# Performance work log

Measured on AMD Instinct MI355X. Metric: run time of the kernel, lower is better.

Reference implementation:

```python
import jax, jax.numpy as jnp
import numpy as np

EPS = 1e-20  # MaskSoftmax epsilon
S, T, B, H, V = 64, 64, 128, 1024, 32000


def _attn(s, h, u, mask, sa_w, sa_b, a1_w, a1_b):
    # Bahdanau attention with mask-softmax over the source (dim 0)
    t = jnp.tanh(s @ sa_w + sa_b + u)               # [S,B,H]
    e = jnp.einsum('sbh,h->sb', t, a1_w) + a1_b     # [S,B]
    x = jnp.exp(e - jnp.max(e, axis=0, keepdims=True)) * mask
    alpha = x / (jnp.sum(x, axis=0, keepdims=True) + EPS)
    return jnp.einsum('sb,sbh->bh', alpha, h)       # [B,H]


def _gru(x, h, ym, W, U, b, C=None, c=None):
    xg = x @ W + b
    if C is not None:
        xg = xg + c @ C
    hg = h @ U
    xz, xr, xh = jnp.split(xg, 3, axis=-1)
    hz, hr, hh = jnp.split(hg, 3, axis=-1)
    z = jax.nn.sigmoid(xz + hz)
    r = jax.nn.sigmoid(xr + hr)
    hn = (1.0 - z) * h + z * jnp.tanh(xh + r * hh)
    m = ym[:, None]
    return m * hn + (1.0 - m) * h


def _forward(ys, xs_h, uh, xs_mask, ys_mask, s_tm1, emb, sa_w, sa_b, a1_w, a1_b,
             ha_w, ha_b, W1, U1, b1, W2, U2, C2, b2,
             ua1_w, ua1_b, ua2_w, ua2_b, ls_w, ls_b, ly_w, ly_b, lc_w, lc_b):
    ys_e = emb[ys]                                              # [T,B,H]
    btg_uh = jnp.einsum('sbh,hk->sbk', xs_h, ha_w) + ha_b        # [S,B,H]

    def step(s, inp):
        y_e, ym = inp
        s_above = _gru(y_e, s, ym, W1, U1, b1)                   # gru1
        a1 = _attn(s_above, xs_h, uh, xs_mask, sa_w, sa_b, a1_w, a1_b)
        a2 = _attn(s_above, xs_h, btg_uh, xs_mask, sa_w, sa_b, a1_w, a1_b)
        s_t = _gru(a1, s_above, ym, W2, U2, b2, C2, a2)          # gru2 with extra ctx
        g = jax.nn.sigmoid(a1 @ ua1_w + ua1_b + a2 @ ua2_w + ua2_b)
        att = g * a1 + (1.0 - g) * a2                            # gated fusion
        logit = s_t @ ls_w + ls_b + y_e @ ly_w + ly_b + att @ lc_w + lc_b  # [B,2H]
        logit = jnp.max(logit.reshape(logit.shape[0], -1, 2), axis=-1)     # maxout
        return s_t, logit

    _, logits = jax.lax.scan(step, s_tm1, (ys_e, ys_mask))       # [T,B,H]
    return logits * ys_mask[:, :, None]


def setup_inputs():
    key = jax.random.key(0)
    ks = jax.random.split(key, 20)
    rn = lambda k, sh, s=0.02: jax.random.normal(k, sh, jnp.float32) * s
    inp = {}
    inp['ys'] = jax.random.randint(ks[0], (T, B), 0, V)
    inp['xs_h'] = jax.random.normal(ks[1], (S, B, H), jnp.float32)
    inp['uh'] = jax.random.normal(ks[2], (S, B, H), jnp.float32)
    inp['xs_mask'] = jnp.ones((S, B), jnp.float32)
    inp['ys_mask'] = jnp.ones((T, B), jnp.float32)
    inp['s_tm1'] = rn(ks[3], (B, H), 1.0)
    emb = rn(ks[4], (V, H), 1.0)
    inp['emb'] = emb.at[0].set(0.0)  # padding_idx = 0
    inp['sa_w'] = rn(ks[5], (H, H)); inp['sa_b'] = jnp.zeros((H,), jnp.float32)
    inp['a1_w'] = rn(ks[6], (H,));   inp['a1_b'] = jnp.zeros((), jnp.float32)
    inp['ha_w'] = rn(ks[7], (H, H)); inp['ha_b'] = jnp.zeros((H,), jnp.float32)
    inp['W1'] = rn(ks[8], (H, 3 * H)); inp['U1'] = rn(ks[9], (H, 3 * H)); inp['b1'] = jnp.zeros((3 * H,), jnp.float32)
    inp['W2'] = rn(ks[10], (H, 3 * H)); inp['U2'] = rn(ks[11], (H, 3 * H)); inp['C2'] = rn(ks[12], (H, 3 * H)); inp['b2'] = jnp.zeros((3 * H,), jnp.float32)
    inp['ua1_w'] = rn(ks[13], (H, H)); inp['ua1_b'] = jnp.zeros((H,), jnp.float32)
    inp['ua2_w'] = rn(ks[14], (H, H)); inp['ua2_b'] = jnp.zeros((H,), jnp.float32)
    inp['ls_w'] = rn(ks[15], (H, 2 * H)); inp['ls_b'] = jnp.zeros((2 * H,), jnp.float32)
    inp['ly_w'] = rn(ks[16], (H, 2 * H)); inp['ly_b'] = jnp.zeros((2 * H,), jnp.float32)
    inp['lc_w'] = rn(ks[17], (H, 2 * H)); inp['lc_b'] = jnp.zeros((2 * H,), jnp.float32)
    return inp


def reference(ys, xs_h, uh, xs_mask, ys_mask, s_tm1, emb, sa_w, sa_b, a1_w, a1_b,
              ha_w, ha_b, W1, U1, b1, W2, U2, C2, b2,
              ua1_w, ua1_b, ua2_w, ua2_b, ls_w, ls_b, ly_w, ly_b, lc_w, lc_b):
    return _forward(ys, xs_h, uh, xs_mask, ys_mask, s_tm1, emb, sa_w, sa_b, a1_w, a1_b,
                    ha_w, ha_b, W1, U1, b1, W2, U2, C2, b2,
                    ua1_w, ua1_b, ua2_w, ua2_b, ls_w, ls_b, ly_w, ly_b, lc_w, lc_b)
```

## Files before the change

kernel.cpp:

```cpp
#include <hip/hip_runtime.h>
#include <hip/hip_bf16.h>
#include <cstddef>
#include <cstdint>

#define Sdim 64
#define Tdim 64
#define Bdim 128
#define Hdim 1024
#define H3 3072
#define TB (Tdim * Bdim)
#define SB (Sdim * Bdim)
#define NWG 256

typedef __attribute__((ext_vector_type(4))) float f32x4;
typedef __attribute__((ext_vector_type(8))) short bf16x8;

__device__ __forceinline__ float rcpf(float x) { return __builtin_amdgcn_rcpf(x); }
__device__ __forceinline__ float sigf(float x) { return rcpf(1.0f + __expf(-x)); }
__device__ __forceinline__ float tanh_fast(float x) {
  x = fminf(fmaxf(x, -15.0f), 15.0f);
  float t = __expf(2.0f * x);
  return (t - 1.0f) * rcpf(t + 1.0f);
}
__device__ __forceinline__ float bl(uint32_t u) { return __uint_as_float(u << 16); }
__device__ __forceinline__ float bh(uint32_t u) { return __uint_as_float(u & 0xffff0000u); }
__device__ __forceinline__ float b2f(uint16_t v) { return __uint_as_float((uint32_t)v << 16); }
__device__ __forceinline__ uint16_t f2b(float f) {
  __hip_bfloat16 h = __float2bfloat16(f);
  return *reinterpret_cast<uint16_t*>(&h);
}

__device__ __forceinline__ uint32_t ald32(const void* p) {
  return __hip_atomic_load((const uint32_t*)p, __ATOMIC_RELAXED, __HIP_MEMORY_SCOPE_AGENT);
}
__device__ __forceinline__ unsigned long long ald64(const void* p) {
  return __hip_atomic_load((const unsigned long long*)p, __ATOMIC_RELAXED, __HIP_MEMORY_SCOPE_AGENT);
}
__device__ __forceinline__ void ast32(void* p, uint32_t v) {
  __hip_atomic_store((uint32_t*)p, v, __ATOMIC_RELAXED, __HIP_MEMORY_SCOPE_AGENT);
}
__device__ __forceinline__ void ast64(void* p, unsigned long long v) {
  __hip_atomic_store((unsigned long long*)p, v, __ATOMIC_RELAXED, __HIP_MEMORY_SCOPE_AGENT);
}
__device__ __forceinline__ float aldf(const void* p) { return __uint_as_float(ald32(p)); }
__device__ __forceinline__ void astf(void* p, float v) { ast32(p, __float_as_uint(v)); }
__device__ __forceinline__ uint4 ald128(const void* p) {
  unsigned long long a = ald64(p);
  unsigned long long b = ald64((const char*)p + 8);
  uint4 r;
  r.x = (uint32_t)a; r.y = (uint32_t)(a >> 32);
  r.z = (uint32_t)b; r.w = (uint32_t)(b >> 32);
  return r;
}

struct MDesc {
  const uint16_t* A0; const uint16_t* B0;
  const uint16_t* A1; const uint16_t* B1;
  const uint16_t* A2; const uint16_t* B2;
  const float* bias0; const float* bias1; const float* bias2;
  float* C;
  int M, N, K;
};

template<int BM, int BN, int MODE>
__global__ __launch_bounds__(256) void mgemm(MDesc d, const float* __restrict__ ymask,
                                             float* __restrict__ outp)
{
  const int nb = blockIdx.x * BN;
  const int mb = blockIdx.y * BM;
  if (nb >= d.N || mb >= d.M) return;

  __shared__ char lds[(BM + BN) * 128];
  char* As = lds;
  char* Bs = lds + BM * 128;

  const int t = threadIdx.x;
  const int lane = t & 63;
  const int wid = t >> 6;
  const int wm = wid >> 1, wn = wid & 1;
  constexpr int WM = BM / 2, WN = BN / 2;
  constexpr int MR = WM / 16, NR = WN / 16;
  constexpr int CA = BM / 32;
  constexpr int CB = BN / 32;

  const int arow_base = wm * WM + (lane & 15);
  const int brow_base = wn * WN + (lane & 15);
  const int akb = (lane >> 4) * 16;
  const int axA = (arow_base & 7) << 4;
  const int axB = (brow_base & 7) << 4;

  f32x4 acc[MR][NR];
  #pragma unroll
  for (int m = 0; m < MR; ++m)
    #pragma unroll
    for (int n = 0; n < NR; ++n)
      acc[m][n] = (f32x4){0.f, 0.f, 0.f, 0.f};

  const int K = d.K;
  const int nkt = K / 64;

  #pragma unroll 1
  for (int p = 0; p < 3; ++p) {
    const uint16_t* A = (p == 0) ? d.A0 : (p == 1 ? d.A1 : d.A2);
    const uint16_t* B = (p == 0) ? d.B0 : (p == 1 ? d.B1 : d.B2);
    if (A == nullptr) break;

    const char* gA[CA]; int lA[CA];
    const char* gB[CB]; int lB[CB];
    #pragma unroll
    for (int c = 0; c < CA; ++c) {
      int i = c * 256 + t, row = i >> 3, kb = (i & 7) * 16;
      gA[c] = (const char*)A + (size_t)(mb + row) * K * 2 + kb;
      lA[c] = row * 128 + (kb ^ ((row & 7) << 4));
    }
    #pragma unroll
    for (int c = 0; c < CB; ++c) {
      int i = c * 256 + t, row = i >> 3, kb = (i & 7) * 16;
      gB[c] = (const char*)B + (size_t)(nb + row) * K * 2 + kb;
      lB[c] = row * 128 + (kb ^ ((row & 7) << 4));
    }

    uint4 ra[CA], rb[CB];
    #pragma unroll
    for (int c = 0; c < CA; ++c) ra[c] = *(const uint4*)gA[c];
    #pragma unroll
    for (int c = 0; c < CB; ++c) rb[c] = *(const uint4*)gB[c];

    for (int kk = 0; kk < nkt; ++kk) {
      __syncthreads();
      #pragma unroll
      for (int c = 0; c < CA; ++c) *(uint4*)(As + lA[c]) = ra[c];
      #pragma unroll
      for (int c = 0; c < CB; ++c) *(uint4*)(Bs + lB[c]) = rb[c];
      __syncthreads();
      if (kk + 1 < nkt) {
        #pragma unroll
        for (int c = 0; c < CA; ++c) ra[c] = *(const uint4*)(gA[c] + (size_t)(kk + 1) * 128);
        #pragma unroll
        for (int c = 0; c < CB; ++c) rb[c] = *(const uint4*)(gB[c] + (size_t)(kk + 1) * 128);
      }
      #pragma unroll
      for (int ks = 0; ks < 2; ++ks) {
        bf16x8 av[MR], bv[NR];
        #pragma unroll
        for (int m = 0; m < MR; ++m) {
          int row = arow_base + m * 16;
          av[m] = *(const bf16x8*)(As + row * 128 + ((ks * 64 + akb) ^ axA));
        }
        #pragma unroll
        for (int n = 0; n < NR; ++n) {
          int row = brow_base + n * 16;
          bv[n] = *(const bf16x8*)(Bs + row * 128 + ((ks * 64 + akb) ^ axB));
        }
        #pragma unroll
        for (int m = 0; m < MR; ++m)
          #pragma unroll
          for (int n = 0; n < NR; ++n)
            acc[m][n] = __builtin_amdgcn_mfma_f32_16x16x32_bf16(av[m], bv[n], acc[m][n], 0, 0, 0);
      }
    }
  }

  const int cm = (lane >> 4) * 4;
  const int cn = lane & 15;
  #pragma unroll
  for (int n = 0; n < NR; ++n) {
    int col = nb + wn * WN + n * 16 + cn;
    float bias = 0.f;
    if (d.bias0) bias += d.bias0[col];
    if (d.bias1) bias += d.bias1[col];
    if (d.bias2) bias += d.bias2[col];
    #pragma unroll
    for (int m = 0; m < MR; ++m) {
      #pragma unroll
      for (int j = 0; j < 4; ++j) {
        int row = mb + wm * WM + m * 16 + cm + j;
        float v = acc[m][n][j] + bias;
        if (MODE == 1) {
          ((uint16_t*)d.C)[(size_t)row * d.N + col] = f2b(v);
        } else {
          float o = __shfl_xor(v, 1);
          if (!(lane & 1))
            outp[(size_t)row * (d.N / 2) + (col >> 1)] = fmaxf(v, o) * ymask[row];
        }
      }
    }
  }
}

static inline MDesc mk(const uint16_t* A0, const uint16_t* B0,
                       const uint16_t* A1, const uint16_t* B1,
                       const uint16_t* A2, const uint16_t* B2,
                       const float* b0, const float* b1, const float* b2,
                       float* C, int M, int N, int K)
{
  MDesc d;
  d.A0 = A0; d.B0 = B0; d.A1 = A1; d.B1 = B1; d.A2 = A2; d.B2 = B2;
  d.bias0 = b0; d.bias1 = b1; d.bias2 = b2;
  d.C = C; d.M = M; d.N = N; d.K = K;
  return d;
}

__global__ __launch_bounds__(256) void transpose_bf16_k(const float* __restrict__ in,
                                                        uint16_t* __restrict__ out,
                                                        int K, int N)
{
  __shared__ float tile[32][33];
  int nx = blockIdx.x * 32, ky = blockIdx.y * 32;
  int tx = threadIdx.x & 31, ty = threadIdx.x >> 5;
  #pragma unroll
  for (int i = 0; i < 4; ++i)
    tile[ty + i * 8][tx] = in[(size_t)(ky + ty + i * 8) * N + nx + tx];
  __syncthreads();
  #pragma unroll
  for (int i = 0; i < 4; ++i)
    out[(size_t)(nx + ty + i * 8) * K + ky + tx] = f2b(tile[tx][ty + i * 8]);
}

__global__ __launch_bounds__(256) void ptranspose_k(const float* __restrict__ in,
                                                    uint16_t* __restrict__ out,
                                                    int K, int N)
{
  __shared__ float tile[32][33];
  int nx = blockIdx.x * 32, ky = blockIdx.y * 32;
  int tx = threadIdx.x & 31, ty = threadIdx.x >> 5;
  #pragma unroll
  for (int i = 0; i < 4; ++i)
    tile[ty + i * 8][tx] = in[(size_t)(ky + ty + i * 8) * N + nx + tx];
  __syncthreads();
  #pragma unroll
  for (int i = 0; i < 4; ++i) {
    int n = nx + ty + i * 8;
    int h = n & 1023, g = n >> 10;
    int np = (h >> 4) * 48 + g * 16 + (h & 15);
    out[(size_t)np * K + ky + tx] = f2b(tile[tx][ty + i * 8]);
  }
}

__global__ __launch_bounds__(256) void pack_k(const float* __restrict__ b1,
                                              const float* __restrict__ b2,
                                              float* __restrict__ b1p,
                                              float* __restrict__ b2p,
                                              int* __restrict__ bar)
{
  int i = blockIdx.x * 256 + threadIdx.x;
  if (i < 1024) bar[i] = 0;
  if (i < H3) {
    int g = (i >> 4) % 3, hblk = i / 48, hi = i & 15;
    int n = g * 1024 + hblk * 16 + hi;
    b1p[i] = b1[n];
    b2p[i] = b2[n];
  }
}

__global__ __launch_bounds__(256) void cvt_bf16_k(const float* __restrict__ in,
                                                  uint16_t* __restrict__ out)
{
  int gid = blockIdx.x * 256 + threadIdx.x;
  float4 v = ((const float4*)in)[gid];
  uint2 o;
  o.x = (uint32_t)f2b(v.x) | ((uint32_t)f2b(v.y) << 16);
  o.y = (uint32_t)f2b(v.z) | ((uint32_t)f2b(v.w) << 16);
  ((uint2*)out)[gid] = o;
}

__global__ __launch_bounds__(256) void embed_k(const int* __restrict__ ys,
                                               const float* __restrict__ emb,
                                               uint16_t* __restrict__ ys_e)
{
  int gid = blockIdx.x * 256 + threadIdx.x;
  int h4 = gid & 255;
  int tb = gid >> 8;
  int tok = ys[tb];
  float4 v = ((const float4*)emb)[(size_t)tok * 256 + h4];
  uint2 o;
  o.x = (uint32_t)f2b(v.x) | ((uint32_t)f2b(v.y) << 16);
  o.y = (uint32_t)f2b(v.z) | ((uint32_t)f2b(v.w) << 16);
  ((uint2*)ys_e)[gid] = o;
}

struct ScanArgs {
  const uint16_t *U1p, *W2p, *C2p, *U2p;
  const uint16_t *sawt, *ua1t, *ua2t;
  const uint16_t *xw1p;
  const uint16_t *uh_bf, *btg_bf, *xs_bf;
  const uint16_t *stm1_bf;
  const float *s_tm1, *ys_mask, *xs_mask, *a1w, *a1b, *sa_b;
  const float *b2p, *ua1_b, *ua2_b;
  float *sf0, *sf1, *sab_f, *qbuf, *e1, *e2, *c1f, *c2f, *ahg;
  uint16_t *sab_bf, *c1b, *c2b, *shist_bf, *att_bf;
  int *bar;
};

__device__ __forceinline__ void gsync(int* bar, int gen, int wg) {
  __syncthreads();
  if (threadIdx.x == 0) {
    asm volatile("s_waitcnt vmcnt(0)" ::: "memory");
    int old = __hip_atomic_fetch_add(bar + (wg & 15) * 32, 1,
                                     __ATOMIC_RELAXED, __HIP_MEMORY_SCOPE_AGENT);
    if (old == gen * 16 - 1) {
      int ro = __hip_atomic_fetch_add(bar + 512, 1,
                                      __ATOMIC_RELAXED, __HIP_MEMORY_SCOPE_AGENT);
      if (ro == gen * 16 - 1)
        __hip_atomic_store(bar + 544, gen, __ATOMIC_RELAXED, __HIP_MEMORY_SCOPE_AGENT);
    }
    while (__hip_atomic_load(bar + 544, __ATOMIC_RELAXED, __HIP_MEMORY_SCOPE_AGENT) < gen)
      __builtin_amdgcn_s_sleep(2);
    asm volatile("s_waitcnt vmcnt(0)" ::: "memory");
  }
  __syncthreads();
}

#define HS1 16384
#define HS2 12288
#define HS6 16384
#define HS5 32768

__global__ __launch_bounds__(256, 1) void scan2_k(ScanArgs a) {
  const int wg = blockIdx.x;
  const int t = threadIdx.x;
  const int lane = t & 63, w = t >> 6;
  const int r15 = lane & 15;
  const int akb = (lane >> 4) * 16;
  __shared__ char lds[64 * 1024];
  int gen = 0;

  float wv[16];
  {
    const float* wp = a.a1w + lane * 16;
    #pragma unroll
    for (int j = 0; j < 16; ++j) wv[j] = wp[j];
  }
  const float abv = a.a1b[0];

  const int b34 = wg & 127;
  const uint16_t* src34 = (wg < 128) ? a.uh_bf : a.btg_bf;
  const size_t s34_base = ((size_t)(w * 16) * Bdim + b34) * 1024 + lane * 16;
  float* cf34 = (wg < 128) ? a.c1f : a.c2f;
  uint16_t* cb34 = (wg < 128) ? a.c1b : a.c2b;
  const uint16_t* xp34 = a.xs_bf + (size_t)b34 * 1024 + t * 4;

  const int bh6 = (wg & 127) >> 6, hb6 = wg & 63;
  const char* ga6[4]; int la6[4];
  {
    #pragma unroll
    for (int c = 0; c < 4; ++c) {
      int i = c * 256 + t;
      int row = i >> 3, kb = (i & 7) * 16;
      if (i < 512) {
        ga6[c] = (const char*)a.sab_bf + ((size_t)(bh6 * 64 + row) * 1024) * 2 + kb;
      } else if (i < 896) {
        int j2 = i - 512; int row2 = j2 >> 3;
        ga6[c] = (const char*)a.U2p + ((size_t)(hb6 * 48 + row2) * 1024) * 2 + kb;
        row = 64 + row2;
      } else {
        ga6[c] = (const char*)a.U2p + kb;
      }
      la6[c] = row * 128 + (kb ^ ((row & 7) << 4));
    }
  }

  const int bh5 = (wg & 127) >> 6, hblk = wg & 63;
  const char* ga5[8]; int la5[8];
  {
    #pragma unroll
    for (int c = 0; c < 8; ++c) {
      int i = c * 256 + t;
      int kb = (i & 7) * 16, grow = i >> 3;
      const char* gp;
      if (grow < 64)       gp = (const char*)a.c1b  + ((size_t)(bh5 * 64 + grow)        * 1024) * 2;
      else if (grow < 128) gp = (const char*)a.c2b  + ((size_t)(bh5 * 64 + grow - 64)   * 1024) * 2;
      else if (grow < 176) gp = (const char*)a.W2p  + ((size_t)(hblk * 48 + grow - 128) * 1024) * 2;
      else if (grow < 224) gp = (const char*)a.C2p  + ((size_t)(hblk * 48 + grow - 176) * 1024) * 2;
      else if (grow < 240) gp = (const char*)a.ua1t + ((size_t)(hblk * 16 + grow - 224) * 1024) * 2;
      else                 gp = (const char*)a.ua2t + ((size_t)(hblk * 16 + grow - 240) * 1024) * 2;
      ga5[c] = gp + kb;
      la5[c] = grow * 128 + (kb ^ ((grow & 7) << 4));
    }
  }

  for (int step = 0; step < Tdim; ++step) {
    const uint16_t* sprev_bf = step ? (a.shist_bf + (size_t)(step - 1) * Bdim * Hdim) : a.stm1_bf;
    const float* sprev_f = (step == 0) ? a.s_tm1 : ((step & 1) ? a.sf0 : a.sf1);
    float* snext_f = (step & 1) ? a.sf1 : a.sf0;
    const float* ymt = a.ys_mask + (size_t)step * Bdim;
    uint16_t* shist_t = a.shist_bf + (size_t)step * Bdim * Hdim;
    uint16_t* att_t = a.att_bf + (size_t)step * Bdim * Hdim;
    const uint16_t* xw1t = a.xw1p + (size_t)step * Bdim * H3;

    uint4 v6w0, v6w1, v6w2, v6w3;

    if (wg < 128) {
      const char* ga1[4]; int la1[4];
      #pragma unroll
      for (int c = 0; c < 4; ++c) {
        int i = c * 256 + t;
        int row = i >> 3, kb = (i & 7) * 16;
        if (i < 512) {
          ga1[c] = (const char*)sprev_bf + ((size_t)(bh5 * 64 + row) * 1024) * 2 + kb;
        } else if (i < 896) {
          int j2 = i - 512; int row2 = j2 >> 3;
          ga1[c] = (const char*)a.U1p + ((size_t)(hblk * 48 + row2) * 1024) * 2 + kb;
          row = 64 + row2;
        } else {
          ga1[c] = (const char*)a.U1p + kb;
        }
        la1[c] = row * 128 + (kb ^ ((row & 7) << 4));
      }
      f32x4 ac0 = {0.f,0.f,0.f,0.f}, ac1 = ac0, ac2 = ac0;
      const int arow = w * 16 + r15;
      const int axA = (arow & 7) << 4;
      const int axB = (r15 & 7) << 4;
      uint4 rA[4], rB[4];
      auto ld1 = [&](uint4* r, int tile) {
        #pragma unroll
        for (int c = 0; c < 4; ++c)
          r[c] = (c < 2) ? ald128(ga1[c] + (size_t)tile * 128)
                         : *(const uint4*)(ga1[c] + (size_t)tile * 128);
      };
      auto st1 = [&](const uint4* r, int half) {
        char* base = lds + half * HS1;
        #pragma unroll
        for (int c = 0; c < 4; ++c) *(uint4*)(base + la1[c]) = r[c];
      };
      auto cp1 = [&](int half) {
        const char* base = lds + half * HS1;
        #pragma unroll
        for (int ks = 0; ks < 2; ++ks) {
          int ko = ks * 64 + akb;
          bf16x8 av = *(const bf16x8*)(base + arow * 128 + (ko ^ axA));
          bf16x8 b0 = *(const bf16x8*)(base + (64 + r15) * 128 + (ko ^ axB));
          bf16x8 b1 = *(const bf16x8*)(base + (80 + r15) * 128 + (ko ^ axB));
          bf16x8 b2 = *(const bf16x8*)(base + (96 + r15) * 128 + (ko ^ axB));
          ac0 = __builtin_amdgcn_mfma_f32_16x16x32_bf16(av, b0, ac0, 0, 0, 0);
          ac1 = __builtin_amdgcn_mfma_f32_16x16x32_bf16(av, b1, ac1, 0, 0, 0);
          ac2 = __builtin_amdgcn_mfma_f32_16x16x32_bf16(av, b2, ac2, 0, 0, 0);
        }
      };
      ld1(rA, 0); ld1(rB, 1);
      st1(rA, 0);
      #pragma unroll 1
      for (int kk2 = 0; kk2 < 8; ++kk2) {
        __syncthreads();
        st1(rB, 1);
        if (kk2 < 7) ld1(rA, 2 * kk2 + 2);
        cp1(0);
        __syncthreads();
        if (kk2 < 7) { st1(rA, 0); ld1(rB, 2 * kk2 + 3); }
        cp1(1);
      }
      const int hgl = hblk * 16 + r15;
      const int bbase = bh5 * 64 + w * 16 + ((lane >> 4) << 2);
      #pragma unroll
      for (int j = 0; j < 4; ++j) {
        int b = bbase + j;
        size_t xr_ = (size_t)b * H3 + hblk * 48 + r15;
        float xz = b2f(xw1t[xr_]);
        float xr = b2f(xw1t[xr_ + 16]);
        float xh = b2f(xw1t[xr_ + 32]);
        float hp = aldf(sprev_f + b * 1024 + hgl);
        float z = sigf(xz + ac0[j]);
        float r = sigf(xr + ac1[j]);
        float hn = (1.f - z) * hp + z * tanh_fast(xh + r * ac2[j]);
        float m = ymt[b];
        float o = m * hn + (1.f - m) * hp;
        astf(a.sab_f + b * 1024 + hgl, o);
        uint32_t me = f2b(o);
        uint32_t other = (uint32_t)__shfl_xor((int)me, 1);
        if (!(lane & 1))
          ast32((char*)a.sab_bf + ((size_t)b * 1024 + hgl) * 2, me | (other << 16));
      }
    } else {
      v6w0 = *(const uint4*)ga6[2];
      v6w1 = *(const uint4*)ga6[3];
      v6w2 = *(const uint4*)(ga6[2] + 128);
      v6w3 = *(const uint4*)(ga6[3] + 128);
    }
    gsync(a.bar, ++gen, wg);

    if (wg < 64) {
      const int bh2 = wg >> 5, nblk = wg & 31;
      const char* ga2[3]; int la2[3];
      #pragma unroll
      for (int c = 0; c < 3; ++c) {
        int i = c * 256 + t;
        int row, kb = (i & 7) * 16;
        if (i < 512) {
          row = i >> 3;
          ga2[c] = (const char*)a.sab_bf + ((size_t)(bh2 * 64 + row) * 1024) * 2 + kb;
        } else {
          int j2 = i - 512; int row2 = j2 >> 3;
          ga2[c] = (const char*)a.sawt + ((size_t)(nblk * 32 + row2) * 1024) * 2 + kb;
          row = 64 + row2;
        }
        la2[c] = row * 128 + (kb ^ ((row & 7) << 4));
      }
      f32x4 q0 = {0.f,0.f,0.f,0.f}, q1 = q0;
      const int arow = w * 16 + r15;
      const int axA = (arow & 7) << 4;
      const int axB = (r15 & 7) << 4;
      uint4 rA[3], rB[3];
      auto ld2 = [&](uint4* r, int tile) {
        #pragma unroll
        for (int c = 0; c < 3; ++c)
          r[c] = (c < 2) ? ald128(ga2[c] + (size_t)tile * 128)
                         : *(const uint4*)(ga2[c] + (size_t)tile * 128);
      };
      auto st2 = [&](const uint4* r, int half) {
        char* base = lds + half * HS2;
        #pragma unroll
        for (int c = 0; c < 3; ++c) *(uint4*)(base + la2[c]) = r[c];
      };
      auto cp2 = [&](int half) {
        const char* base = lds + half * HS2;
        #pragma unroll
        for (int ks = 0; ks < 2; ++ks) {
          int ko = ks * 64 + akb;
          bf16x8 av = *(const bf16x8*)(base + arow * 128 + (ko ^ axA));
          bf16x8 b0 = *(const bf16x8*)(base + (64 + r15) * 128 + (ko ^ axB));
          bf16x8 b1 = *(const bf16x8*)(base + (80 + r15) * 128 + (ko ^ axB));
          q0 = __builtin_amdgcn_mfma_f32_16x16x32_bf16(av, b0, q0, 0, 0, 0);
          q1 = __builtin_amdgcn_mfma_f32_16x16x32_bf16(av, b1, q1, 0, 0, 0);
        }
      };
      ld2(rA, 0); ld2(rB, 1);
      st2(rA, 0);
      #pragma unroll 1
      for (int kk2 = 0; kk2 < 8; ++kk2) {
        __syncthreads();
        st2(rB, 1);
        if (kk2 < 7) ld2(rA, 2 * kk2 + 2);
        cp2(0);
        __syncthreads();
        if (kk2 < 7) { st2(rA, 0); ld2(rB, 2 * kk2 + 3); }
        cp2(1);
      }
      #pragma unroll
      for (int n = 0; n < 2; ++n) {
        int col = nblk * 32 + n * 16 + r15;
        float sb = a.sa_b[col];
        #pragma unroll
        for (int j = 0; j < 4; ++j) {
          int b = bh2 * 64 + w * 16 + ((lane >> 4) << 2) + j;
          astf(a.qbuf + b * 1024 + col, (n ? q1[j] : q0[j]) + sb);
        }
      }
    } else if (wg >= 128) {
      f32x4 ac0 = {0.f,0.f,0.f,0.f}, ac1 = ac0, ac2 = ac0;
      const int arow = w * 16 + r15;
      const int axA = (arow & 7) << 4;
      const int axB = (r15 & 7) << 4;
      uint4 rA[4], rB[4];
      auto ld6 = [&](uint4* r, int tile) {
        #pragma unroll
        for (int c = 0; c < 4; ++c)
          r[c] = (c < 2) ? ald128(ga6[c] + (size_t)tile * 128)
                         : *(const uint4*)(ga6[c] + (size_t)tile * 128);
      };
      auto st6 = [&](const uint4* r, int half) {
        char* base = lds + half * HS6;
        #pragma unroll
        for (int c = 0; c < 4; ++c) *(uint4*)(base + la6[c]) = r[c];
      };
      auto cp6 = [&](int half) {
        const char* base = lds + half * HS6;
        #pragma unroll
        for (int ks = 0; ks < 2; ++ks) {
          int ko = ks * 64 + akb;
          bf16x8 av = *(const bf16x8*)(base + arow * 128 + (ko ^ axA));
          bf16x8 b0 = *(const bf16x8*)(base + (64 + r15) * 128 + (ko ^ axB));
          bf16x8 b1 = *(const bf16x8*)(base + (80 + r15) * 128 + (ko ^ axB));
          bf16x8 b2 = *(const bf16x8*)(base + (96 + r15) * 128 + (ko ^ axB));
          ac0 = __builtin_amdgcn_mfma_f32_16x16x32_bf16(av, b0, ac0, 0, 0, 0);
          ac1 = __builtin_amdgcn_mfma_f32_16x16x32_bf16(av, b1, ac1, 0, 0, 0);
          ac2 = __builtin_amdgcn_mfma_f32_16x16x32_bf16(av, b2, ac2, 0, 0, 0);
        }
      };
      rA[0] = ald128(ga6[0]);       rA[1] = ald128(ga6[1]);
      rA[2] = v6w0;                 rA[3] = v6w1;
      rB[0] = ald128(ga6[0] + 128); rB[1] = ald128(ga6[1] + 128);
      rB[2] = v6w2;                 rB[3] = v6w3;
      st6(rA, 0);
      #pragma unroll 1
      for (int kk2 = 0; kk2 < 8; ++kk2) {
        __syncthreads();
        st6(rB, 1);
        if (kk2 < 7) ld6(rA, 2 * kk2 + 2);
        cp6(0);
        __syncthreads();
        if (kk2 < 7) { st6(rA, 0); ld6(rB, 2 * kk2 + 3); }
        cp6(1);
      }
      const int bbase6 = bh6 * 64 + w * 16 + ((lane >> 4) << 2);
      #pragma unroll
      for (int j = 0; j < 4; ++j) {
        int b = bbase6 + j;
        float* ap = a.ahg + (size_t)b * H3 + hb6 * 48 + r15;
        astf(ap, ac0[j]);
        astf(ap + 16, ac1[j]);
        astf(ap + 32, ac2[j]);
      }
    }
    uint4 pa0 = *(const uint4*)(src34 + s34_base);
    uint4 pa1 = *(const uint4*)(src34 + s34_base + 8);
    gsync(a.bar, ++gen, wg);

    {
      float* e_lds = (float*)lds;
      float qv[16];
      const float* qp = a.qbuf + (size_t)b34 * 1024 + lane * 16;
      #pragma unroll
      for (int k2 = 0; k2 < 8; ++k2) {
        unsigned long long q2 = ald64(qp + k2 * 2);
        qv[2 * k2]     = __uint_as_float((uint32_t)q2);
        qv[2 * k2 + 1] = __uint_as_float((uint32_t)(q2 >> 32));
      }
      auto score = [&](uint4 u0, uint4 u1, int si) {
        float pv = 0.f;
        uint32_t uu[8] = {u0.x,u0.y,u0.z,u0.w,u1.x,u1.y,u1.z,u1.w};
        #pragma unroll
        for (int k = 0; k < 8; ++k) {
          pv += wv[2*k]   * tanh_fast(qv[2*k]   + bl(uu[k]));
          pv += wv[2*k+1] * tanh_fast(qv[2*k+1] + bh(uu[k]));
        }
        #pragma unroll
        for (int off = 32; off > 0; off >>= 1) pv += __shfl_xor(pv, off);
        if (lane == 0) e_lds[w * 16 + si] = pv + abv;
      };
      uint4 pb0, pb1;
      {
        const uint16_t* np = src34 + s34_base + (size_t)Bdim * 1024;
        pb0 = *(const uint4*)np; pb1 = *(const uint4*)(np + 8);
      }
      #pragma unroll 1
      for (int s2 = 0; s2 < 8; ++s2) {
        {
          int si = 2 * s2;
          uint4 u0 = pa0, u1 = pa1;
          if (s2 < 7) {
            const uint16_t* np = src34 + s34_base + (size_t)(si + 2) * Bdim * 1024;
            pa0 = *(const uint4*)np; pa1 = *(const uint4*)(np + 8);
          }
          score(u0, u1, si);
        }
        {
          int si = 2 * s2 + 1;
          uint4 u0 = pb0, u1 = pb1;
          if (s2 < 7) {
            const uint16_t* np = src34 + s34_base + (size_t)(si + 2) * Bdim * 1024;
            pb0 = *(const uint4*)np; pb1 = *(const uint4*)(np + 8);
          }
          score(u0, u1, si);
        }
      }
      __syncthreads();
      if (w == 0) {
        float vv = e_lds[lane];
        float mx = vv;
        #pragma unroll
        for (int off = 32; off > 0; off >>= 1) mx = fmaxf(mx, __shfl_xor(mx, off));
        float x = __expf(vv - mx) * a.xs_mask[lane * Bdim + b34];
        float sm = x;
        #pragma unroll
        for (int off = 32; off > 0; off >>= 1) sm += __shfl_xor(sm, off);
        e_lds[lane] = x * rcpf(sm + 1e-20f);
      }
      __syncthreads();
      float s0 = 0.f, s1 = 0.f, s2 = 0.f, s3 = 0.f;
      #pragma unroll 8
      for (int s = 0; s < Sdim; ++s) {
        unsigned long long u = *(const unsigned long long*)(xp34 + (size_t)s * Bdim * 1024);
        float aa = e_lds[s];
        s0 += aa * bl((uint32_t)u);
        s1 += aa * bh((uint32_t)u);
        s2 += aa * bl((uint32_t)(u >> 32));
        s3 += aa * bh((uint32_t)(u >> 32));
      }
      size_t o = (size_t)b34 * 1024 + t * 4;
      ast64(cf34 + o,     (unsigned long long)__float_as_uint(s0)
                        | ((unsigned long long)__float_as_uint(s1) << 32));
      ast64(cf34 + o + 2, (unsigned long long)__float_as_uint(s2)
                        | ((unsigned long long)__float_as_uint(s3) << 32));
      unsigned long long pb = (unsigned long long)f2b(s0)
                            | ((unsigned long long)f2b(s1) << 16)
                            | ((unsigned long long)f2b(s2) << 32)
                            | ((unsigned long long)f2b(s3) << 48);
      ast64((char*)cb34 + o * 2, pb);
    }
    uint4 v5w[8];
    if (wg < 128) {
      #pragma unroll
      for (int c = 4; c < 8; ++c) {
        v5w[c - 4] = *(const uint4*)ga5[c];
        v5w[c]     = *(const uint4*)(ga5[c] + 128);
      }
    }
    gsync(a.bar, ++gen, wg);

    if (wg < 128) {
      f32x4 ax0 = {0.f,0.f,0.f,0.f}, ax1 = ax0, ax2 = ax0, ag = ax0;
      uint4 rA[8], rB[8];
      auto ld5 = [&](uint4* r, int tile) {
        #pragma unroll
        for (int c = 0; c < 8; ++c)
          r[c] = (c < 4) ? ald128(ga5[c] + (size_t)tile * 128)
                         : *(const uint4*)(ga5[c] + (size_t)tile * 128);
      };
      auto st5 = [&](const uint4* r, int half) {
        char* base = lds + half * HS5;
        #pragma unroll
        for (int c = 0; c < 8; ++c) *(uint4*)(base + la5[c]) = r[c];
      };
      auto cp5 = [&](int half) {
        const char* base = lds + half * HS5;
        #pragma unroll
        for (int ks = 0; ks < 2; ++ks) {
          const int ko = ks * 64 + akb;
          #define LD(row_) (*(const bf16x8*)(base + (row_) * 128 + (ko ^ (((row_) & 7) << 4))))
          bf16x8 a1v = LD(w * 16 + r15);
          bf16x8 a2v = LD(64 + w * 16 + r15);
          bf16x8 bw0 = LD(128 + r15), bw1 = LD(144 + r15), bw2 = LD(160 + r15);
          bf16x8 bc0 = LD(176 + r15), bc1 = LD(192 + r15), bc2 = LD(208 + r15);
          bf16x8 g1v = LD(224 + r15), g2v = LD(240 + r15);
          #undef LD
          ax0 = __builtin_amdgcn_mfma_f32_16x16x32_bf16(a1v, bw0, ax0, 0, 0, 0);
          ax0 = __builtin_amdgcn_mfma_f32_16x16x32_bf16(a2v, bc0, ax0, 0, 0, 0);
          ax1 = __builtin_amdgcn_mfma_f32_16x16x32_bf16(a1v, bw1, ax1, 0, 0, 0);
          ax1 = __builtin_amdgcn_mfma_f32_16x16x32_bf16(a2v, bc1, ax1, 0, 0, 0);
          ax2 = __builtin_amdgcn_mfma_f32_16x16x32_bf16(a1v, bw2, ax2, 0, 0, 0);
          ax2 = __builtin_amdgcn_mfma_f32_16x16x32_bf16(a2v, bc2, ax2, 0, 0, 0);
          ag  = __builtin_amdgcn_mfma_f32_16x16x32_bf16(a1v, g1v, ag, 0, 0, 0);
          ag  = __builtin_amdgcn_mfma_f32_16x16x32_bf16(a2v, g2v, ag, 0, 0, 0);
        }
      };
      #pragma unroll
      for (int c = 0; c < 4; ++c) {
        rA[c] = ald128(ga5[c]);
        rB[c] = ald128(ga5[c] + 128);
      }
      #pragma unroll
      for (int c = 4; c < 8; ++c) { rA[c] = v5w[c - 4]; rB[c] = v5w[c]; }
      st5(rA, 0);
      #pragma unroll 1
      for (int kk2 = 0; kk2 < 8; ++kk2) {
        __syncthreads();
        st5(rB, 1);
        if (kk2 < 7) ld5(rA, 2 * kk2 + 2);
        cp5(0);
        __syncthreads();
        if (kk2 < 7) { st5(rA, 0); ld5(rB, 2 * kk2 + 3); }
        cp5(1);
      }
      const int hgl = hblk * 16 + r15;
      float bz  = a.b2p[hblk * 48 + r15];
      float brr = a.b2p[hblk * 48 + 16 + r15];
      float bhh = a.b2p[hblk * 48 + 32 + r15];
      float gb  = a.ua1_b[hgl] + a.ua2_b[hgl];
      const int bbase = bh5 * 64 + w * 16 + ((lane >> 4) << 2);
      float ahz[4], ahr[4], ahh[4], hpv[4], c1v[4], c2v[4];
      #pragma unroll
      for (int j = 0; j < 4; ++j) {
        int b = bbase + j;
        const float* ap = a.ahg + (size_t)b * H3 + hblk * 48 + r15;
        ahz[j] = aldf(ap);
        ahr[j] = aldf(ap + 16);
        ahh[j] = aldf(ap + 32);
        hpv[j] = aldf(a.sab_f + (size_t)b * 1024 + hgl);
        c1v[j] = aldf(a.c1f + (size_t)b * 1024 + hgl);
        c2v[j] = aldf(a.c2f + (size_t)b * 1024 + hgl);
      }
      #pragma unroll
      for (int j = 0; j < 4; ++j) {
        int b = bbase + j;
        float hp = hpv[j];
        float z = sigf(ax0[j] + bz + ahz[j]);
        float r = sigf(ax1[j] + brr + ahr[j]);
        float hn = (1.f - z) * hp + z * tanh_fast(ax2[j] + bhh + r * ahh[j]);
        float m = ymt[b];
        float st = m * hn + (1.f - m) * hp;
        astf(snext_f + b * 1024 + hgl, st);
        uint32_t me = f2b(st);
        uint32_t other = (uint32_t)__shfl_xor((int)me, 1);
        if (!(lane & 1))
          ast32((char*)shist_t + ((size_t)b * 1024 + hgl) * 2, me | (other << 16));
        float g = sigf(ag[j] + gb);
        float att = g * c1v[j] + (1.f - g) * c2v[j];
        att_t[(size_t)b * 1024 + hgl] = f2b(att);
      }
    }
    gsync(a.bar, ++gen, wg);
  }
}

extern "C" void kernel_launch(void* const* d_in, const int* in_sizes, int n_in,
                              void* d_out, int out_size, void* d_ws, size_t ws_size,
                              hipStream_t stream)
{
  const int*   ys      = (const int*)  d_in[0];
  const float* xs_h    = (const float*)d_in[1];
  const float* uh      = (const float*)d_in[2];
  const float* xs_mask = (const float*)d_in[3];
  const float* ys_mask = (const float*)d_in[4];
  const float* s_tm1   = (const float*)d_in[5];
  const float* emb     = (const float*)d_in[6];
  const float* sa_w    = (const float*)d_in[7];
  const float* sa_b    = (const float*)d_in[8];
  const float* a1_w    = (const float*)d_in[9];
  const float* a1_b    = (const float*)d_in[10];
  const float* ha_w    = (const float*)d_in[11];
  const float* ha_b    = (const float*)d_in[12];
  const float* W1      = (const float*)d_in[13];
  const float* U1      = (const float*)d_in[14];
  const float* b1      = (const float*)d_in[15];
  const float* W2      = (const float*)d_in[16];
  const float* U2      = (const float*)d_in[17];
  const float* C2      = (const float*)d_in[18];
  const float* b2      = (const float*)d_in[19];
  const float* ua1_w   = (const float*)d_in[20];
  const float* ua1_b   = (const float*)d_in[21];
  const float* ua2_w   = (const float*)d_in[22];
  const float* ua2_b   = (const float*)d_in[23];
  const float* ls_w    = (const float*)d_in[24];
  const float* ls_b    = (const float*)d_in[25];
  const float* ly_w    = (const float*)d_in[26];
  const float* ly_b    = (const float*)d_in[27];
  const float* lc_w    = (const float*)d_in[28];
  const float* lc_b    = (const float*)d_in[29];
  (void)in_sizes; (void)n_in; (void)out_size; (void)ws_size;

  float* out = (float*)d_out;

  char* wp = (char*)d_ws;
  auto alloc = [&](size_t bytes) { char* r = wp; wp += (bytes + 255) & ~(size_t)255; return r; };

  uint16_t* W1p  = (uint16_t*)alloc((size_t)H3 * Hdim * 2);
  uint16_t* U1p  = (uint16_t*)alloc((size_t)H3 * Hdim * 2);
  uint16_t* W2p  = (uint16_t*)alloc((size_t)H3 * Hdim * 2);
  uint16_t* U2p  = (uint16_t*)alloc((size_t)H3 * Hdim * 2);
  uint16_t* C2p  = (uint16_t*)alloc((size_t)H3 * Hdim * 2);
  uint16_t* sawt = (uint16_t*)alloc((size_t)Hdim * Hdim * 2);
  uint16_t* hawt = (uint16_t*)alloc((size_t)Hdim * Hdim * 2);
  uint16_t* ua1t = (uint16_t*)alloc((size_t)Hdim * Hdim * 2);
  uint16_t* ua2t = (uint16_t*)alloc((size_t)Hdim * Hdim * 2);
  uint16_t* lst  = (uint16_t*)alloc((size_t)2048 * Hdim * 2);
  uint16_t* lyt  = (uint16_t*)alloc((size_t)2048 * Hdim * 2);
  uint16_t* lct  = (uint16_t*)alloc((size_t)2048 * Hdim * 2);
  float* b1p = (float*)alloc((size_t)H3 * 4);
  float* b2p = (float*)alloc((size_t)H3 * 4);
  int* bar   = (int*)alloc(4096);
  uint16_t* uh_bf   = (uint16_t*)alloc((size_t)SB * Hdim * 2);
  uint16_t* xs_bf   = (uint16_t*)alloc((size_t)SB * Hdim * 2);
  uint16_t* btg_bf  = (uint16_t*)alloc((size_t)SB * Hdim * 2);
  uint16_t* ys_e_bf = (uint16_t*)alloc((size_t)TB * Hdim * 2);
  uint16_t* xw1p    = (uint16_t*)alloc((size_t)TB * H3 * 2);
  uint16_t* shist_bf= (uint16_t*)alloc((size_t)TB * Hdim * 2);
  uint16_t* att_bf  = (uint16_t*)alloc((size_t)TB * Hdim * 2);
  uint16_t* stm1_bf = (uint16_t*)alloc((size_t)Bdim * Hdim * 2);
  float* sab_f = (float*)alloc((size_t)Bdim * Hdim * 4);
  uint16_t* sab_bf = (uint16_t*)alloc((size_t)Bdim * Hdim * 2);
  float* qbuf = (float*)alloc((size_t)Bdim * Hdim * 4);
  float* c1f  = (float*)alloc((size_t)Bdim * Hdim * 4);
  float* c2f  = (float*)alloc((size_t)Bdim * Hdim * 4);
  uint16_t* c1b = (uint16_t*)alloc((size_t)Bdim * Hdim * 2);
  uint16_t* c2b = (uint16_t*)alloc((size_t)Bdim * Hdim * 2);
  float* e1 = (float*)alloc((size_t)SB * 4);
  float* e2 = (float*)alloc((size_t)SB * 4);
  float* sf0 = (float*)alloc((size_t)Bdim * Hdim * 4);
  float* sf1 = (float*)alloc((size_t)Bdim * Hdim * 4);
  float* ahg = (float*)alloc((size_t)Bdim * H3 * 4);

  pack_k<<<12, 256, 0, stream>>>(b1, b2, b1p, b2p, bar);

  auto ptr3 = [&](const float* in, uint16_t* o) {
    ptranspose_k<<<dim3(H3 / 32, Hdim / 32), 256, 0, stream>>>(in, o, Hdim, H3);
  };
  ptr3(W1, W1p); ptr3(U1, U1p); ptr3(W2, W2p); ptr3(U2, U2p); ptr3(C2, C2p);

  auto tr = [&](const float* in, uint16_t* o, int K, int N) {
    transpose_bf16_k<<<dim3(N / 32, K / 32), 256, 0, stream>>>(in, o, K, N);
  };
  tr(sa_w, sawt, Hdim, Hdim); tr(ha_w, hawt, Hdim, Hdim);
  tr(ua1_w, ua1t, Hdim, Hdim); tr(ua2_w, ua2t, Hdim, Hdim);
  tr(ls_w, lst, Hdim, 2048); tr(ly_w, lyt, Hdim, 2048); tr(lc_w, lct, Hdim, 2048);

  cvt_bf16_k<<<(SB * Hdim / 4) / 256, 256, 0, stream>>>(uh, uh_bf);
  cvt_bf16_k<<<(SB * Hdim / 4) / 256, 256, 0, stream>>>(xs_h, xs_bf);
  cvt_bf16_k<<<(Bdim * Hdim / 4) / 256, 256, 0, stream>>>(s_tm1, stm1_bf);
  embed_k<<<(TB * Hdim / 4) / 256, 256, 0, stream>>>(ys, emb, ys_e_bf);

  {
    MDesc d = mk(ys_e_bf, W1p, 0, 0, 0, 0, b1p, 0, 0, (float*)xw1p, TB, H3, Hdim);
    mgemm<128, 128, 1><<<dim3(H3 / 128, TB / 128), 256, 0, stream>>>(d, nullptr, nullptr);
  }
  {
    MDesc d = mk(xs_bf, hawt, 0, 0, 0, 0, ha_b, 0, 0, (float*)btg_bf, SB, Hdim, Hdim);
    mgemm<128, 128, 1><<<dim3(Hdim / 128, SB / 128), 256, 0, stream>>>(d, nullptr, nullptr);
  }

  ScanArgs sa;
  sa.U1p = U1p; sa.W2p = W2p; sa.C2p = C2p; sa.U2p = U2p;
  sa.sawt = sawt; sa.ua1t = ua1t; sa.ua2t = ua2t;
  sa.xw1p = xw1p;
  sa.uh_bf = uh_bf; sa.btg_bf = btg_bf; sa.xs_bf = xs_bf;
  sa.stm1_bf = stm1_bf;
  sa.s_tm1 = s_tm1; sa.ys_mask = ys_mask; sa.xs_mask = xs_mask;
  sa.a1w = a1_w; sa.a1b = a1_b; sa.sa_b = sa_b;
  sa.b2p = b2p; sa.ua1_b = ua1_b; sa.ua2_b = ua2_b;
  sa.sf0 = sf0; sa.sf1 = sf1; sa.sab_f = sab_f; sa.qbuf = qbuf;
  sa.e1 = e1; sa.e2 = e2; sa.c1f = c1f; sa.c2f = c2f; sa.ahg = ahg;
  sa.sab_bf = sab_bf; sa.c1b = c1b; sa.c2b = c2b;
  sa.shist_bf = shist_bf; sa.att_bf = att_bf;
  sa.bar = bar;
  scan2_k<<<NWG, 256, 0, stream>>>(sa);

  {
    MDesc d = mk(shist_bf, lst, ys_e_bf, lyt, att_bf, lct, ls_b, ly_b, lc_b,
                 nullptr, TB, 2048, Hdim);
    mgemm<128, 128, 2><<<dim3(2048 / 128, TB / 128), 256, 0, stream>>>(d, ys_mask, out);
  }
}
```

Before: 5.119 ms.

## Split-K GRU phases across idle workgroup pairs with flag handoff

Gives the previously idle upper 128 workgroups half of the K range for the GRU1 and GRU2/gate GEMMs in each scan step. They write fp32 partial accumulators to a global buffer and signal per-pair flags, and the lower workgroup spins on the flag, adds the partials and runs the epilogue. This halves the serial MMA loop length in two phases of the recurrent scan. It adds global partial-sum traffic, a pairwise spin-wait, and drops the phase-6 weight prefetch those workgroups previously did.

```diff
diff --git a/kernel.cpp b/kernel.cpp
--- a/kernel.cpp
+++ b/kernel.cpp
@@ -52,6 +52,9 @@
   r.z = (uint32_t)b; r.w = (uint32_t)(b >> 32);
   return r;
 }
+#define PK2(x, y) ((unsigned long long)__float_as_uint(x) | ((unsigned long long)__float_as_uint(y) << 32))
+__device__ __forceinline__ float ulo(unsigned long long u) { return __uint_as_float((uint32_t)u); }
+__device__ __forceinline__ float uhi(unsigned long long u) { return __uint_as_float((uint32_t)(u >> 32)); }
 
 struct MDesc {
   const uint16_t* A0; const uint16_t* B0;
@@ -288,6 +291,7 @@
   const float *s_tm1, *ys_mask, *xs_mask, *a1w, *a1b, *sa_b;
   const float *b2p, *ua1_b, *ua2_b;
   float *sf0, *sf1, *sab_f, *qbuf, *e1, *e2, *c1f, *c2f, *ahg;
+  float *p1part, *p5part;
   uint16_t *sab_bf, *c1b, *c2b, *shist_bf, *att_bf;
   int *bar;
 };
@@ -315,6 +319,7 @@
 #define HS2 12288
 #define HS6 16384
 #define HS5 32768
+
 
 __global__ __launch_bounds__(256, 1) void scan2_k(ScanArgs a) {
   const int wg = blockIdx.x;
@@ -361,6 +366,9 @@
   }
 
   const int bh5 = (wg & 127) >> 6, hblk = wg & 63;
+  const int pairid = wg & 127;
+  const int koff = (wg < 128) ? 0 : 8;
+
   const char* ga5[8]; int la5[8];
   {
     #pragma unroll
@@ -374,10 +382,13 @@
       else if (grow < 224) gp = (const char*)a.C2p  + ((size_t)(hblk * 48 + grow - 176) * 1024) * 2;
       else if (grow < 240) gp = (const char*)a.ua1t + ((size_t)(hblk * 16 + grow - 224) * 1024) * 2;
       else                 gp = (const char*)a.ua2t + ((size_t)(hblk * 16 + grow - 240) * 1024) * 2;
-      ga5[c] = gp + kb;
+      ga5[c] = gp + kb + (size_t)koff * 128;
       la5[c] = grow * 128 + (kb ^ ((grow & 7) << 4));
     }
   }
+
+  unsigned long long* p1p = (unsigned long long*)a.p1part + (size_t)pairid * 1536 + t;
+  unsigned long long* p5p = (unsigned long long*)a.p5part + (size_t)pairid * 2048 + t;
 
   for (int step = 0; step < Tdim; ++step) {
     const uint16_t* sprev_bf = step ? (a.shist_bf + (size_t)(step - 1) * Bdim * Hdim) : a.stm1_bf;
@@ -388,9 +399,7 @@
     uint16_t* att_t = a.att_bf + (size_t)step * Bdim * Hdim;
     const uint16_t* xw1t = a.xw1p + (size_t)step * Bdim * H3;
 
-    uint4 v6w0, v6w1, v6w2, v6w3;
-
-    if (wg < 128) {
+    {
       const char* ga1[4]; int la1[4];
       #pragma unroll
       for (int c = 0; c < 4; ++c) {
@@ -405,6 +414,7 @@
         } else {
           ga1[c] = (const char*)a.U1p + kb;
         }
+        ga1[c] += (size_t)koff * 128;
         la1[c] = row * 128 + (kb ^ ((row & 7) << 4));
       }
       f32x4 ac0 = {0.f,0.f,0.f,0.f}, ac1 = ac0, ac2 = ac0;
@@ -440,41 +450,61 @@
       ld1(rA, 0); ld1(rB, 1);
       st1(rA, 0);
       #pragma unroll 1
-      for (int kk2 = 0; kk2 < 8; ++kk2) {
+      for (int kk2 = 0; kk2 < 4; ++kk2) {
         __syncthreads();
         st1(rB, 1);
-        if (kk2 < 7) ld1(rA, 2 * kk2 + 2);
+        if (kk2 < 3) ld1(rA, 2 * kk2 + 2);
         cp1(0);
         __syncthreads();
-        if (kk2 < 7) { st1(rA, 0); ld1(rB, 2 * kk2 + 3); }
+        if (kk2 < 3) { st1(rA, 0); ld1(rB, 2 * kk2 + 3); }
         cp1(1);
       }
-      const int hgl = hblk * 16 + r15;
-      const int bbase = bh5 * 64 + w * 16 + ((lane >> 4) << 2);
-      #pragma unroll
-      for (int j = 0; j < 4; ++j) {
-        int b = bbase + j;
-        size_t xr_ = (size_t)b * H3 + hblk * 48 + r15;
-        float xz = b2f(xw1t[xr_]);
-        float xr = b2f(xw1t[xr_ + 16]);
-        float xh = b2f(xw1t[xr_ + 32]);
-        float hp = aldf(sprev_f + b * 1024 + hgl);
-        float z = sigf(xz + ac0[j]);
-        float r = sigf(xr + ac1[j]);
-        float hn = (1.f - z) * hp + z * tanh_fast(xh + r * ac2[j]);
-        float m = ymt[b];
-        float o = m * hn + (1.f - m) * hp;
-        astf(a.sab_f + b * 1024 + hgl, o);
-        uint32_t me = f2b(o);
-        uint32_t other = (uint32_t)__shfl_xor((int)me, 1);
-        if (!(lane & 1))
-          ast32((char*)a.sab_bf + ((size_t)b * 1024 + hgl) * 2, me | (other << 16));
-      }
-    } else {
-      v6w0 = *(const uint4*)ga6[2];
-      v6w1 = *(const uint4*)ga6[3];
-      v6w2 = *(const uint4*)(ga6[2] + 128);
-      v6w3 = *(const uint4*)(ga6[3] + 128);
+      if (wg >= 128) {
+        ast64(p1p +    0, PK2(ac0[0], ac0[1]));
+        ast64(p1p +  256, PK2(ac0[2], ac0[3]));
+        ast64(p1p +  512, PK2(ac1[0], ac1[1]));
+        ast64(p1p +  768, PK2(ac1[2], ac1[3]));
+        ast64(p1p + 1024, PK2(ac2[0], ac2[1]));
+        ast64(p1p + 1280, PK2(ac2[2], ac2[3]));
+        __syncthreads();
+        if (t == 0)
+          __hip_atomic_store(a.bar + 600 + pairid, step + 1,
+                             __ATOMIC_RELAXED, __HIP_MEMORY_SCOPE_AGENT);
+      } else {
+        if (t == 0) {
+          while (__hip_atomic_load(a.bar + 600 + pairid,
+                                   __ATOMIC_RELAXED, __HIP_MEMORY_SCOPE_AGENT) < step + 1)
+            __builtin_amdgcn_s_sleep(1);
+        }
+        __syncthreads();
+        unsigned long long u0 = ald64(p1p), u1 = ald64(p1p + 256),
+                           u2 = ald64(p1p + 512), u3 = ald64(p1p + 768),
+                           u4 = ald64(p1p + 1024), u5 = ald64(p1p + 1280);
+        ac0[0] += ulo(u0); ac0[1] += uhi(u0); ac0[2] += ulo(u1); ac0[3] += uhi(u1);
+        ac1[0] += ulo(u2); ac1[1] += uhi(u2); ac1[2] += ulo(u3); ac1[3] += uhi(u3);
+        ac2[0] += ulo(u4); ac2[1] += uhi(u4); ac2[2] += ulo(u5); ac2[3] += uhi(u5);
+        const int hgl = hblk * 16 + r15;
+        const int bbase = bh5 * 64 + w * 16 + ((lane >> 4) << 2);
+        #pragma unroll
+        for (int j = 0; j < 4; ++j) {
+          int b = bbase + j;
+          size_t xr_ = (size_t)b * H3 + hblk * 48 + r15;
+          float xz = b2f(xw1t[xr_]);
+          float xr = b2f(xw1t[xr_ + 16]);
+          float xh = b2f(xw1t[xr_ + 32]);
+          float hp = aldf(sprev_f + b * 1024 + hgl);
+          float z = sigf(xz + ac0[j]);
+          float r = sigf(xr + ac1[j]);
+          float hn = (1.f - z) * hp + z * tanh_fast(xh + r * ac2[j]);
+          float m = ymt[b];
+          float o = m * hn + (1.f - m) * hp;
+          astf(a.sab_f + b * 1024 + hgl, o);
+          uint32_t me = f2b(o);
+          uint32_t other = (uint32_t)__shfl_xor((int)me, 1);
+          if (!(lane & 1))
+            ast32((char*)a.sab_bf + ((size_t)b * 1024 + hgl) * 2, me | (other << 16));
+        }
+      }
     }
     gsync(a.bar, ++gen, wg);
 
@@ -576,10 +606,7 @@
           ac2 = __builtin_amdgcn_mfma_f32_16x16x32_bf16(av, b2, ac2, 0, 0, 0);
         }
       };
-      rA[0] = ald128(ga6[0]);       rA[1] = ald128(ga6[1]);
-      rA[2] = v6w0;                 rA[3] = v6w1;
-      rB[0] = ald128(ga6[0] + 128); rB[1] = ald128(ga6[1] + 128);
-      rB[2] = v6w2;                 rB[3] = v6w3;
+      ld6(rA, 0); ld6(rB, 1);
       st6(rA, 0);
       #pragma unroll 1
       for (int kk2 = 0; kk2 < 8; ++kk2) {
@@ -688,7 +715,7 @@
       ast64((char*)cb34 + o * 2, pb);
     }
     uint4 v5w[8];
-    if (wg < 128) {
+    {
       #pragma unroll
       for (int c = 4; c < 8; ++c) {
         v5w[c - 4] = *(const uint4*)ga5[c];
@@ -697,7 +724,7 @@
     }
     gsync(a.bar, ++gen, wg);
 
-    if (wg < 128) {
+    {
       f32x4 ax0 = {0.f,0.f,0.f,0.f}, ax1 = ax0, ax2 = ax0, ag = ax0;
       uint4 rA[8], rB[8];
       auto ld5 = [&](uint4* r, int tile) {
@@ -742,50 +769,79 @@
       for (int c = 4; c < 8; ++c) { rA[c] = v5w[c - 4]; rB[c] = v5w[c]; }
       st5(rA, 0);
       #pragma unroll 1
-      for (int kk2 = 0; kk2 < 8; ++kk2) {
+      for (int kk2 = 0; kk2 < 4; ++kk2) {
         __syncthreads();
         st5(rB, 1);
-        if (kk2 < 7) ld5(rA, 2 * kk2 + 2);
+        if (kk2 < 3) ld5(rA, 2 * kk2 + 2);
         cp5(0);
         __syncthreads();
-        if (kk2 < 7) { st5(rA, 0); ld5(rB, 2 * kk2 + 3); }
+        if (kk2 < 3) { st5(rA, 0); ld5(rB, 2 * kk2 + 3); }
         cp5(1);
       }
-      const int hgl = hblk * 16 + r15;
-      float bz  = a.b2p[hblk * 48 + r15];
-      float brr = a.b2p[hblk * 48 + 16 + r15];
-      float bhh = a.b2p[hblk * 48 + 32 + r15];
-      float gb  = a.ua1_b[hgl] + a.ua2_b[hgl];
-      const int bbase = bh5 * 64 + w * 16 + ((lane >> 4) << 2);
-      float ahz[4], ahr[4], ahh[4], hpv[4], c1v[4], c2v[4];
-      #pragma unroll
-      for (int j = 0; j < 4; ++j) {
-        int b = bbase + j;
-        const float* ap = a.ahg + (size_t)b * H3 + hblk * 48 + r15;
-        ahz[j] = aldf(ap);
-        ahr[j] = aldf(ap + 16);
-        ahh[j] = aldf(ap + 32);
-        hpv[j] = aldf(a.sab_f + (size_t)b * 1024 + hgl);
-        c1v[j] = aldf(a.c1f + (size_t)b * 1024 + hgl);
-        c2v[j] = aldf(a.c2f + (size_t)b * 1024 + hgl);
-      }
-      #pragma unroll
-      for (int j = 0; j < 4; ++j) {
-        int b = bbase + j;
-        float hp = hpv[j];
-        float z = sigf(ax0[j] + bz + ahz[j]);
-        float r = sigf(ax1[j] + brr + ahr[j]);
-        float hn = (1.f - z) * hp + z * tanh_fast(ax2[j] + bhh + r * ahh[j]);
-        float m = ymt[b];
-        float st = m * hn + (1.f - m) * hp;
-        astf(snext_f + b * 1024 + hgl, st);
-        uint32_t me = f2b(st);
-        uint32_t other = (uint32_t)__shfl_xor((int)me, 1);
-        if (!(lane & 1))
-          ast32((char*)shist_t + ((size_t)b * 1024 + hgl) * 2, me | (other << 16));
-        float g = sigf(ag[j] + gb);
-        float att = g * c1v[j] + (1.f - g) * c2v[j];
-        att_t[(size_t)b * 1024 + hgl] = f2b(att);
+      if (wg >= 128) {
+        ast64(p5p +    0, PK2(ax0[0], ax0[1]));
+        ast64(p5p +  256, PK2(ax0[2], ax0[3]));
+        ast64(p5p +  512, PK2(ax1[0], ax1[1]));
+        ast64(p5p +  768, PK2(ax1[2], ax1[3]));
+        ast64(p5p + 1024, PK2(ax2[0], ax2[1]));
+        ast64(p5p + 1280, PK2(ax2[2], ax2[3]));
+        ast64(p5p + 1536, PK2(ag[0], ag[1]));
+        ast64(p5p + 1792, PK2(ag[2], ag[3]));
+        __syncthreads();
+        if (t == 0)
+          __hip_atomic_store(a.bar + 728 + pairid, step + 1,
+                             __ATOMIC_RELAXED, __HIP_MEMORY_SCOPE_AGENT);
+      } else {
+        if (t == 0) {
+          while (__hip_atomic_load(a.bar + 728 + pairid,
+                                   __ATOMIC_RELAXED, __HIP_MEMORY_SCOPE_AGENT) < step + 1)
+            __builtin_amdgcn_s_sleep(1);
+        }
+        __syncthreads();
+        unsigned long long u0 = ald64(p5p), u1 = ald64(p5p + 256),
+                           u2 = ald64(p5p + 512), u3 = ald64(p5p + 768),
+                           u4 = ald64(p5p + 1024), u5 = ald64(p5p + 1280),
+                           u6 = ald64(p5p + 1536), u7 = ald64(p5p + 1792);
+        ax0[0] += ulo(u0); ax0[1] += uhi(u0); ax0[2] += ulo(u1); ax0[3] += uhi(u1);
+        ax1[0] += ulo(u2); ax1[1] += uhi(u2); ax1[2] += ulo(u3); ax1[3] += uhi(u3);
+        ax2[0] += ulo(u4); ax2[1] += uhi(u4); ax2[2] += ulo(u5); ax2[3] += uhi(u5);
+        ag[0]  += ulo(u6); ag[1]  += uhi(u6); ag[2]  += ulo(u7); ag[3]  += uhi(u7);
+        const int hgl = hblk * 16 + r15;
+        float bz  = a.b2p[hblk * 48 + r15];
+        float brr = a.b2p[hblk * 48 + 16 + r15];
+        float bhh = a.b2p[hblk * 48 + 32 + r15];
+        float gb  = a.ua1_b[hgl] + a.ua2_b[hgl];
+        const int bbase = bh5 * 64 + w * 16 + ((lane >> 4) << 2);
+        float ahz[4], ahr[4], ahh[4], hpv[4], c1v[4], c2v[4];
+        #pragma unroll
+        for (int j = 0; j < 4; ++j) {
+          int b = bbase + j;
+          const float* ap = a.ahg + (size_t)b * H3 + hblk * 48 + r15;
+          ahz[j] = aldf(ap);
+          ahr[j] = aldf(ap + 16);
+          ahh[j] = aldf(ap + 32);
+          hpv[j] = aldf(a.sab_f + (size_t)b * 1024 + hgl);
+          c1v[j] = aldf(a.c1f + (size_t)b * 1024 + hgl);
+          c2v[j] = aldf(a.c2f + (size_t)b * 1024 + hgl);
+        }
+        #pragma unroll
+        for (int j = 0; j < 4; ++j) {
+          int b = bbase + j;
+          float hp = hpv[j];
+          float z = sigf(ax0[j] + bz + ahz[j]);
+          float r = sigf(ax1[j] + brr + ahr[j]);
+          float hn = (1.f - z) * hp + z * tanh_fast(ax2[j] + bhh + r * ahh[j]);
+          float m = ymt[b];
+          float st = m * hn + (1.f - m) * hp;
+          astf(snext_f + b * 1024 + hgl, st);
+          uint32_t me = f2b(st);
+          uint32_t other = (uint32_t)__shfl_xor((int)me, 1);
+          if (!(lane & 1))
+            ast32((char*)shist_t + ((size_t)b * 1024 + hgl) * 2, me | (other << 16));
+          float g = sigf(ag[j] + gb);
+          float att = g * c1v[j] + (1.f - g) * c2v[j];
+          att_t[(size_t)b * 1024 + hgl] = f2b(att);
+        }
       }
     }
     gsync(a.bar, ++gen, wg);
@@ -868,6 +924,8 @@
   float* sf0 = (float*)alloc((size_t)Bdim * Hdim * 4);
   float* sf1 = (float*)alloc((size_t)Bdim * Hdim * 4);
   float* ahg = (float*)alloc((size_t)Bdim * H3 * 4);
+  float* p1part = (float*)alloc((size_t)128 * 1536 * 8);
+  float* p5part = (float*)alloc((size_t)128 * 2048 * 8);
 
   pack_k<<<12, 256, 0, stream>>>(b1, b2, b1p, b2p, bar);
 
@@ -908,6 +966,7 @@
   sa.b2p = b2p; sa.ua1_b = ua1_b; sa.ua2_b = ua2_b;
   sa.sf0 = sf0; sa.sf1 = sf1; sa.sab_f = sab_f; sa.qbuf = qbuf;
   sa.e1 = e1; sa.e2 = e2; sa.c1f = c1f; sa.c2f = c2f; sa.ahg = ahg;
+  sa.p1part = p1part; sa.p5part = p5part;
   sa.sab_bf = sab_bf; sa.c1b = c1b; sa.c2b = c2b;
   sa.shist_bf = shist_bf; sa.att_bf = att_bf;
   sa.bar = bar;
```

Measured after the change: 4.966 ms. 1.03x faster.
